# Kernel tuning notes

Hardware: AMD Instinct MI355X
Metric: run time of the kernel (lower is better)

Reference implementation:

```python
import jax, jax.numpy as jnp
import numpy as np

HEADS = 8
EMBED = 512
D_K = EMBED // HEADS
B, S = 2, 4096


def setup_inputs() -> dict:
    key = jax.random.key(0)
    ks = jax.random.split(key, 12)
    sc = 1.0 / np.sqrt(EMBED)
    inp = {
        "query": jax.random.normal(ks[0], (B, S, EMBED), jnp.float32),
        "key": jax.random.normal(ks[1], (B, S, EMBED), jnp.float32),
        "value": jax.random.normal(ks[2], (B, S, EMBED), jnp.float32),
        # causal (decoder) mask, broadcast over batch and heads
        "mask": jnp.tril(jnp.ones((S, S), jnp.int32))[None, None, :, :],
        "Wq": jax.random.normal(ks[3], (EMBED, EMBED), jnp.float32) * sc,
        "bq": jnp.zeros((EMBED,), jnp.float32),
        "Wk": jax.random.normal(ks[4], (EMBED, EMBED), jnp.float32) * sc,
        "bk": jnp.zeros((EMBED,), jnp.float32),
        "Wv": jax.random.normal(ks[5], (EMBED, EMBED), jnp.float32) * sc,
        "bv": jnp.zeros((EMBED,), jnp.float32),
        "Wo": jax.random.normal(ks[6], (EMBED, EMBED), jnp.float32) * sc,
        "bo": jnp.zeros((EMBED,), jnp.float32),
    }
    return inp


def reference(query, key, value, mask, Wq, bq, Wk, bk, Wv, bv, Wo, bo):
    b, s, e = query.shape
    # linear projections (torch Linear: x @ W.T + b)
    q = query @ Wq.T + bq
    k = key @ Wk.T + bk
    v = value @ Wv.T + bv
    # [b, h, s, d_k]
    q = q.reshape(b, s, HEADS, D_K).transpose(0, 2, 1, 3)
    k = k.reshape(b, s, HEADS, D_K).transpose(0, 2, 1, 3)
    v = v.reshape(b, s, HEADS, D_K).transpose(0, 2, 1, 3)
    scores = jnp.einsum("bhqd,bhkd->bhqk", q, k) / jnp.sqrt(jnp.float32(D_K))
    scores = jnp.where(mask == 0, jnp.float32(-1e20), scores)
    attn = jax.nn.softmax(scores, axis=-1)  # dropout is identity in eval
    ctx = jnp.einsum("bhqk,bhkd->bhqd", attn, v)
    ctx = ctx.transpose(0, 2, 1, 3).reshape(b, s, e)
    return ctx @ Wo.T + bo
```

## Files before the change

### kernel.cpp

```cpp
#include <hip/hip_runtime.h>
#include <hip/hip_bf16.h>

#define HEADS 8
#define DK    64
#define SEQ   4096
#define EMB   512
#define BATCH 2

using f32x4  = __attribute__((ext_vector_type(4))) float;
using f32x16 = __attribute__((ext_vector_type(16))) float;
using bf16x8 = __attribute__((ext_vector_type(8))) short;
using uint2v = __attribute__((ext_vector_type(2))) uint;

union frg { uint u[4]; bf16x8 v; };

__device__ __forceinline__ ushort f2bf(float f) {
    union { float f; uint32_t u; } x{f};
    uint32_t r = (x.u + 0x7fff + ((x.u >> 16) & 1)) >> 16;
    return (ushort)r;
}

__device__ __forceinline__ float bf2f(ushort u) {
    union { uint u; float f; } x; x.u = ((uint)u) << 16; return x.f;
}

__device__ __forceinline__ uint pk2(float a, float b) {
    __hip_bfloat162 h = __float22bfloat162_rn(make_float2(a, b));
    union { __hip_bfloat162 h; uint u; } c; c.h = h; return c.u;
}

__device__ __forceinline__ uint2v pswap(uint a, uint b) {
    return __builtin_amdgcn_permlane32_swap(a, b, false, false);
}

__device__ __forceinline__ void gld16(const ushort* g, short* l) {
    __builtin_amdgcn_global_load_lds(
        (const __attribute__((address_space(1))) void*)g,
        (__attribute__((address_space(3))) void*)l, 16, 0, 0);
}

__global__ __launch_bounds__(256) void gemm_qkv(
    const float* __restrict__ Aq, const float* __restrict__ Ak, const float* __restrict__ Av,
    const float* __restrict__ Wq, const float* __restrict__ Wk, const float* __restrict__ Wv,
    const float* __restrict__ bq, const float* __restrict__ bk, const float* __restrict__ bv,
    ushort* __restrict__ Qb, ushort* __restrict__ Kb, ushort* __restrict__ Vb)
{
    const int z = blockIdx.z;
    const float* A    = z == 0 ? Aq : z == 1 ? Ak : Av;
    const float* W    = z == 0 ? Wq : z == 1 ? Wk : Wv;
    const float* bias = z == 0 ? bq : z == 1 ? bk : bv;
    ushort* out       = z == 0 ? Qb : z == 1 ? Kb : Vb;
    const float osc   = z == 0 ? 0.125f * 1.44269504089f : 1.0f;

    const int Kd = EMB;
    __shared__ short As[128][40];
    __shared__ short Bs[128][40];

    const int tid = threadIdx.x;
    const int wave = tid >> 6, lane = tid & 63;
    const int wm = wave >> 1, wn = wave & 1;
    const int lr = lane & 15, lg = lane >> 4;
    const int m0 = blockIdx.x * 128, n0 = blockIdx.y * 128;

    f32x4 acc[4][4] = {};

    for (int k0 = 0; k0 < Kd; k0 += 32) {
        #pragma unroll
        for (int i = 0; i < 4; ++i) {
            int idx4 = tid + i * 256;
            int r = idx4 >> 3, c = (idx4 & 7) * 4;
            float4 va = *(const float4*)(A + (size_t)(m0 + r) * Kd + k0 + c);
            ushort4 ha;
            ha.x = f2bf(va.x); ha.y = f2bf(va.y); ha.z = f2bf(va.z); ha.w = f2bf(va.w);
            *(ushort4*)(&As[r][c]) = ha;
            float4 vb2 = *(const float4*)(W + (size_t)(n0 + r) * Kd + k0 + c);
            ushort4 hb;
            hb.x = f2bf(vb2.x); hb.y = f2bf(vb2.y); hb.z = f2bf(vb2.z); hb.w = f2bf(vb2.w);
            *(ushort4*)(&Bs[r][c]) = hb;
        }
        __syncthreads();

        bf16x8 a[4], bfr[4];
        #pragma unroll
        for (int i = 0; i < 4; ++i)
            a[i] = *(const bf16x8*)(&As[wm * 64 + i * 16 + lr][lg * 8]);
        #pragma unroll
        for (int i = 0; i < 4; ++i)
            bfr[i] = *(const bf16x8*)(&Bs[wn * 64 + i * 16 + lr][lg * 8]);

        #pragma unroll
        for (int mi = 0; mi < 4; ++mi)
            #pragma unroll
            for (int ni = 0; ni < 4; ++ni)
                acc[mi][ni] = __builtin_amdgcn_mfma_f32_16x16x32_bf16(
                    a[mi], bfr[ni], acc[mi][ni], 0, 0, 0);
        __syncthreads();
    }

    #pragma unroll
    for (int ni = 0; ni < 4; ++ni) {
        const int n = n0 + wn * 64 + ni * 16 + lr;
        const float bv2 = bias[n];
        #pragma unroll
        for (int mi = 0; mi < 4; ++mi) {
            #pragma unroll
            for (int j = 0; j < 4; ++j) {
                const int mm = m0 + wm * 64 + mi * 16 + lg * 4 + j;
                float v = (acc[mi][ni][j] + bv2) * osc;
                const int b = mm >> 12, s = mm & (SEQ - 1);
                const int h = n >> 6,  d = n & (DK - 1);
                size_t off;
                if (z == 2) off = ((size_t)(b * HEADS + h) * DK  + d) * SEQ + s;
                else        off = ((size_t)(b * HEADS + h) * SEQ + s) * DK + d;
                out[off] = f2bf(v);
            }
        }
    }
}

__global__ __launch_bounds__(256) void gemm_out(
    const ushort* __restrict__ Ab, const float* __restrict__ W,
    const float* __restrict__ bias, float* __restrict__ out)
{
    const int N = EMB, Kd = EMB;
    __shared__ short As[128][40];
    __shared__ short Bs[128][40];

    const int tid = threadIdx.x;
    const int wave = tid >> 6, lane = tid & 63;
    const int wm = wave >> 1, wn = wave & 1;
    const int lr = lane & 15, lg = lane >> 4;
    const int m0 = blockIdx.x * 128, n0 = blockIdx.y * 128;

    f32x4 acc[4][4] = {};

    for (int k0 = 0; k0 < Kd; k0 += 32) {
        #pragma unroll
        for (int i = 0; i < 2; ++i) {
            int idx8 = tid + i * 256;
            int r = idx8 >> 2, c = (idx8 & 3) * 8;
            bf16x8 v = *(const bf16x8*)(Ab + (size_t)(m0 + r) * Kd + k0 + c);
            *(bf16x8*)(&As[r][c]) = v;
        }
        #pragma unroll
        for (int i = 0; i < 4; ++i) {
            int idx4 = tid + i * 256;
            int r = idx4 >> 3, c = (idx4 & 7) * 4;
            float4 v = *(const float4*)(W + (size_t)(n0 + r) * Kd + k0 + c);
            ushort4 hb;
            hb.x = f2bf(v.x); hb.y = f2bf(v.y); hb.z = f2bf(v.z); hb.w = f2bf(v.w);
            *(ushort4*)(&Bs[r][c]) = hb;
        }
        __syncthreads();

        bf16x8 a[4], bfr[4];
        #pragma unroll
        for (int i = 0; i < 4; ++i)
            a[i] = *(const bf16x8*)(&As[wm * 64 + i * 16 + lr][lg * 8]);
        #pragma unroll
        for (int i = 0; i < 4; ++i)
            bfr[i] = *(const bf16x8*)(&Bs[wn * 64 + i * 16 + lr][lg * 8]);

        #pragma unroll
        for (int mi = 0; mi < 4; ++mi)
            #pragma unroll
            for (int ni = 0; ni < 4; ++ni)
                acc[mi][ni] = __builtin_amdgcn_mfma_f32_16x16x32_bf16(
                    a[mi], bfr[ni], acc[mi][ni], 0, 0, 0);
        __syncthreads();
    }

    #pragma unroll
    for (int ni = 0; ni < 4; ++ni) {
        const int n = n0 + wn * 64 + ni * 16 + lr;
        const float bv = bias[n];
        #pragma unroll
        for (int mi = 0; mi < 4; ++mi)
            #pragma unroll
            for (int j = 0; j < 4; ++j) {
                const int mm = m0 + wm * 64 + mi * 16 + lg * 4 + j;
                out[(size_t)mm * N + n] = acc[mi][ni][j] + bv;
            }
    }
}

__global__ __launch_bounds__(256) void merge_ctx(
    const ushort* __restrict__ Opseg, const float* __restrict__ Lseg,
    ushort* __restrict__ ctx)
{
    const int idx = blockIdx.x * 256 + threadIdx.x;
    const int d8  = idx & 7;
    const int row = idx >> 3;
    const int bh  = row >> 12, s = row & (SEQ - 1);
    const int nseg = (2 * (s >> 7) + 2 + 15) >> 4;

    float acc[8] = {};
    float l = 0.f;
    for (int g = 0; g < nseg; ++g) {
        const ushort* p = Opseg + (((size_t)g * 16 + bh) * SEQ + s) * 64 + d8 * 8;
        ushort4 a = *(const ushort4*)(p);
        ushort4 b2 = *(const ushort4*)(p + 4);
        acc[0] += bf2f(a.x);  acc[1] += bf2f(a.y);
        acc[2] += bf2f(a.z);  acc[3] += bf2f(a.w);
        acc[4] += bf2f(b2.x); acc[5] += bf2f(b2.y);
        acc[6] += bf2f(b2.z); acc[7] += bf2f(b2.w);
        l += Lseg[((size_t)g * 16 + bh) * SEQ + s];
    }
    const float rl = 1.0f / l;
    const int b = bh >> 3, h = bh & 7;
    ushort* o = ctx + ((size_t)b * SEQ + s) * EMB + h * 64 + d8 * 8;
    ushort4 r0, r1;
    r0.x = f2bf(acc[0] * rl); r0.y = f2bf(acc[1] * rl);
    r0.z = f2bf(acc[2] * rl); r0.w = f2bf(acc[3] * rl);
    r1.x = f2bf(acc[4] * rl); r1.y = f2bf(acc[5] * rl);
    r1.z = f2bf(acc[6] * rl); r1.w = f2bf(acc[7] * rl);
    *(ushort4*)(o)     = r0;
    *(ushort4*)(o + 4) = r1;
}

__global__ __launch_bounds__(256) void attn12(
    const ushort* __restrict__ Q, const ushort* __restrict__ K,
    const ushort* __restrict__ Vt,
    ushort* __restrict__ Opseg, float* __restrict__ Lseg)
{
    __shared__ short kv[2][2][64][64];

    const int tid  = threadIdx.x;
    const int wave = tid >> 6, lane = tid & 63;
    const int ql = lane & 31, hi = lane >> 5;

    const int bid = blockIdx.x;
    const int xcd = bid & 7;
    const int idx = bid >> 3;
    const int p   = idx & 1;
    const int j   = idx >> 1;
    int qblk, seg;
    if (j < 32)      { qblk = 31 - (j >> 2);      seg = j & 3; }
    else if (j < 56) { int jj = j - 32; int d3 = jj / 3; qblk = 23 - d3; seg = jj - d3 * 3; }
    else if (j < 72) { int jj = j - 56; qblk = 15 - (jj >> 1); seg = jj & 1; }
    else             { qblk = 7 - (j - 72);       seg = 0; }
    const int bh = xcd * 2 + p;

    const int q0b = qblk * 128;
    const int q0w = q0b + wave * 32;
    const int qg  = q0w + ql;

    const int ntchunk = 2 * qblk + 2;
    const int t_begin = seg * 16;
    const int t_end   = min(t_begin + 16, ntchunk);
    const int ntw     = (q0w + 31) / 64 + 1;

    const ushort* Qp = Q  + ((size_t)bh * SEQ + q0w) * DK;
    const ushort* Kp = K  + (size_t)bh * SEQ * DK;
    const ushort* Vp = Vt + (size_t)bh * DK * SEQ;

    bf16x8 qf[4];
    #pragma unroll
    for (int ks = 0; ks < 4; ++ks)
        qf[ks] = *(const bf16x8*)(Qp + ql * DK + ks * 16 + hi * 8);

    bf16x8 ones;
    #pragma unroll
    for (int i = 0; i < 8; ++i) ones[i] = (short)0x3F80;

    f32x16 oa0 = {}, oa1 = {};
    f32x16 oaL = {};

    auto stage = [&](int buf, int t) {
        const int r0 = wave * 16;
        const int rr = lane >> 3;
        const int c  = lane & 7;
        #pragma unroll
        for (int i = 0; i < 2; ++i) {
            int row = r0 + i * 8 + rr;
            gld16(Kp + (size_t)(t * 64 + row) * DK + ((c ^ (row & 7)) << 3),
                  &kv[buf][0][r0 + i * 8][0]);
        }
        #pragma unroll
        for (int i = 0; i < 2; ++i) {
            int row = r0 + i * 8 + rr;
            gld16(Vp + (size_t)row * SEQ + t * 64 + ((c ^ (row & 7)) << 3),
                  &kv[buf][1][r0 + i * 8][0]);
        }
    };

    const int swz = (ql & 7) << 4;

    auto compute = [&](int buf, int kv0, bool masked) {
        const char* kb = (const char*)&kv[buf][0][0][0];
        const char* vb = (const char*)&kv[buf][1][0][0];

        f32x16 s0, s1;
        #pragma unroll
        for (int r = 0; r < 16; ++r) { s0[r] = -20.0f; s1[r] = -20.0f; }
        #pragma unroll
        for (int ks = 0; ks < 4; ++ks) {
            bf16x8 kf = *(const bf16x8*)(kb + ql * 128 + (((ks * 2 + hi) << 4) ^ swz));
            s0 = __builtin_amdgcn_mfma_f32_32x32x16_bf16(kf, qf[ks], s0, 0, 0, 0);
        }
        #pragma unroll
        for (int ks = 0; ks < 4; ++ks) {
            bf16x8 kf = *(const bf16x8*)(kb + (32 + ql) * 128 + (((ks * 2 + hi) << 4) ^ swz));
            s1 = __builtin_amdgcn_mfma_f32_32x32x16_bf16(kf, qf[ks], s1, 0, 0, 0);
        }

        if (masked) {
            #pragma unroll
            for (int r = 0; r < 16; ++r) {
                int kvg = kv0 + (r & 3) + 8 * (r >> 2) + 4 * hi;
                if (kvg      > qg) s0[r] = -3e38f;
                if (kvg + 32 > qg) s1[r] = -3e38f;
            }
        }

        #pragma unroll
        for (int r = 0; r < 16; ++r) {
            s0[r] = exp2f(s0[r]);
            s1[r] = exp2f(s1[r]);
        }

        frg f0, f1, f2, f3;
        {
            uint w01 = pk2(s0[0], s0[1]),   w23 = pk2(s0[2], s0[3]);
            uint w45 = pk2(s0[4], s0[5]),   w67 = pk2(s0[6], s0[7]);
            uint w89 = pk2(s0[8], s0[9]),   wab = pk2(s0[10], s0[11]);
            uint wcd = pk2(s0[12], s0[13]), wef = pk2(s0[14], s0[15]);
            uint2v p0 = pswap(w01, w45), p1 = pswap(w23, w67);
            uint2v p2 = pswap(w89, wcd), p3 = pswap(wab, wef);
            f0.u[0] = p0[0]; f0.u[1] = p1[0]; f0.u[2] = p0[1]; f0.u[3] = p1[1];
            f1.u[0] = p2[0]; f1.u[1] = p3[0]; f1.u[2] = p2[1]; f1.u[3] = p3[1];
        }
        {
            uint w01 = pk2(s1[0], s1[1]),   w23 = pk2(s1[2], s1[3]);
            uint w45 = pk2(s1[4], s1[5]),   w67 = pk2(s1[6], s1[7]);
            uint w89 = pk2(s1[8], s1[9]),   wab = pk2(s1[10], s1[11]);
            uint wcd = pk2(s1[12], s1[13]), wef = pk2(s1[14], s1[15]);
            uint2v p0 = pswap(w01, w45), p1 = pswap(w23, w67);
            uint2v p2 = pswap(w89, wcd), p3 = pswap(wab, wef);
            f2.u[0] = p0[0]; f2.u[1] = p1[0]; f2.u[2] = p0[1]; f2.u[3] = p1[1];
            f3.u[0] = p2[0]; f3.u[1] = p3[0]; f3.u[2] = p2[1]; f3.u[3] = p3[1];
        }

        #pragma unroll
        for (int sl = 0; sl < 4; ++sl) {
            const frg* fp = sl == 0 ? &f0 : sl == 1 ? &f1 : sl == 2 ? &f2 : &f3;
            bf16x8 v0 = *(const bf16x8*)(vb + ql * 128        + (((sl * 2 + hi) << 4) ^ swz));
            bf16x8 v1 = *(const bf16x8*)(vb + (32 + ql) * 128 + (((sl * 2 + hi) << 4) ^ swz));
            oa0 = __builtin_amdgcn_mfma_f32_32x32x16_bf16(v0, fp->v, oa0, 0, 0, 0);
            oa1 = __builtin_amdgcn_mfma_f32_32x32x16_bf16(v1, fp->v, oa1, 0, 0, 0);
            oaL = __builtin_amdgcn_mfma_f32_32x32x16_bf16(ones, fp->v, oaL, 0, 0, 0);
        }
    };

    stage(0, t_begin);
    int cur = 0;
    for (int t = t_begin; t < t_end; ++t) {
        if (t + 1 < t_end) {
            stage(cur ^ 1, t + 1);
            asm volatile("s_waitcnt vmcnt(8)" ::: "memory");
        } else {
            asm volatile("s_waitcnt vmcnt(0)" ::: "memory");
        }
        __builtin_amdgcn_sched_barrier(0);
        __builtin_amdgcn_s_barrier();
        if (t < ntw)
            compute(cur, t * 64, t == ntw - 1);
        __builtin_amdgcn_s_barrier();
        cur ^= 1;
    }

    ushort* orow = Opseg + (((size_t)seg * 16 + bh) * SEQ + qg) * 64;
    #pragma unroll
    for (int g = 0; g < 4; ++g) {
        ushort4 pk;
        pk.x = f2bf(oa0[g * 4 + 0]); pk.y = f2bf(oa0[g * 4 + 1]);
        pk.z = f2bf(oa0[g * 4 + 2]); pk.w = f2bf(oa0[g * 4 + 3]);
        *(ushort4*)(orow + g * 8 + hi * 4) = pk;
    }
    #pragma unroll
    for (int g = 0; g < 4; ++g) {
        ushort4 pk;
        pk.x = f2bf(oa1[g * 4 + 0]); pk.y = f2bf(oa1[g * 4 + 1]);
        pk.z = f2bf(oa1[g * 4 + 2]); pk.w = f2bf(oa1[g * 4 + 3]);
        *(ushort4*)(orow + 32 + g * 8 + hi * 4) = pk;
    }
    if (hi == 0)
        Lseg[((size_t)seg * 16 + bh) * SEQ + qg] = oaL[0];
}

extern "C" void kernel_launch(void* const* d_in, const int* in_sizes, int n_in,
                              void* d_out, int out_size, void* d_ws, size_t ws_size,
                              hipStream_t stream) {
    const float* query = (const float*)d_in[0];
    const float* key   = (const float*)d_in[1];
    const float* value = (const float*)d_in[2];
    const float* Wq = (const float*)d_in[4];
    const float* bq = (const float*)d_in[5];
    const float* Wk = (const float*)d_in[6];
    const float* bk = (const float*)d_in[7];
    const float* Wv = (const float*)d_in[8];
    const float* bv = (const float*)d_in[9];
    const float* Wo = (const float*)d_in[10];
    const float* bo = (const float*)d_in[11];

    const size_t MK = (size_t)BATCH * SEQ * EMB;
    ushort* Qb = (ushort*)d_ws;
    ushort* Kb = Qb + MK;
    ushort* Vb = Kb + MK;
    ushort* Opseg = Vb + MK;
    float*  Lseg  = (float*)(Opseg + (size_t)4 * 16 * SEQ * DK);
    ushort* Cb = Qb;

    gemm_qkv<<<dim3(64, 4, 3), 256, 0, stream>>>(query, key, value,
                                                 Wq, Wk, Wv, bq, bk, bv,
                                                 Qb, Kb, Vb);
    attn12<<<dim3(1280), 256, 0, stream>>>(Qb, Kb, Vb, Opseg, Lseg);
    merge_ctx<<<dim3(2048), 256, 0, stream>>>(Opseg, Lseg, Cb);
    gemm_out<<<dim3(64, 4), 256, 0, stream>>>(Cb, Wo, bo, (float*)d_out);
}
```

Measured before the change: 146.1 us.

## Fuse split-KV merge into output GEMM and load QKV fp32 tiles via LDS DMA

The separate merge_ctx kernel is removed; the output projection GEMM now sums the per-segment partial outputs and normalizers while loading its A tile, which saves one launch and the ctx round trip through memory. The QKV projection GEMM now streams fp32 tiles straight into XOR-swizzled shared memory with global_load_lds and converts them to bf16 when reading fragments. In exchange, each of the 4 column blocks of the output GEMM repeats the merge, and the merge loop inside the GEMM main loop adds latency there. The fp32 LDS tiles also double the shared memory footprint.

```diff
diff --git a/kernel.cpp b/kernel.cpp
--- a/kernel.cpp
+++ b/kernel.cpp
@@ -39,7 +39,13 @@
         (__attribute__((address_space(3))) void*)l, 16, 0, 0);
 }
 
-__global__ __launch_bounds__(256) void gemm_qkv(
+__device__ __forceinline__ void gld16f(const float* g, float* l) {
+    __builtin_amdgcn_global_load_lds(
+        (const __attribute__((address_space(1))) void*)g,
+        (__attribute__((address_space(3))) void*)l, 16, 0, 0);
+}
+
+__global__ __launch_bounds__(256) void gemm_qkv2(
     const float* __restrict__ Aq, const float* __restrict__ Ak, const float* __restrict__ Av,
     const float* __restrict__ Wq, const float* __restrict__ Wk, const float* __restrict__ Wv,
     const float* __restrict__ bq, const float* __restrict__ bk, const float* __restrict__ bv,
@@ -52,7 +58,90 @@
     ushort* out       = z == 0 ? Qb : z == 1 ? Kb : Vb;
     const float osc   = z == 0 ? 0.125f * 1.44269504089f : 1.0f;
 
-    const int Kd = EMB;
+    __shared__ __align__(16) float As[128][32];
+    __shared__ __align__(16) float Bs[128][32];
+
+    const int tid = threadIdx.x;
+    const int wave = tid >> 6, lane = tid & 63;
+    const int wm = wave >> 1, wn = wave & 1;
+    const int lr = lane & 15, lg = lane >> 4;
+    const int rr = lane >> 3, cc = lane & 7;
+    const int m0 = blockIdx.x * 128, n0 = blockIdx.y * 128;
+
+    f32x4 acc[4][4] = {};
+
+    for (int k0 = 0; k0 < EMB; k0 += 32) {
+        #pragma unroll
+        for (int i = 0; i < 4; ++i) {
+            int row = wave * 32 + i * 8 + rr;
+            gld16f(A + (size_t)(m0 + row) * EMB + k0 + ((cc ^ (row & 7)) << 2),
+                   &As[wave * 32 + i * 8][0]);
+            gld16f(W + (size_t)(n0 + row) * EMB + k0 + ((cc ^ (row & 7)) << 2),
+                   &Bs[wave * 32 + i * 8][0]);
+        }
+        asm volatile("s_waitcnt vmcnt(0)" ::: "memory");
+        __builtin_amdgcn_s_barrier();
+
+        const char* ab = (const char*)&As[0][0];
+        const char* bb = (const char*)&Bs[0][0];
+        bf16x8 a[4], b[4];
+        #pragma unroll
+        for (int i = 0; i < 4; ++i) {
+            int row = wm * 64 + i * 16 + lr;
+            f32x4 lo = *(const f32x4*)(ab + row * 128 + (((2 * lg) ^ (row & 7)) << 4));
+            f32x4 hi = *(const f32x4*)(ab + row * 128 + (((2 * lg + 1) ^ (row & 7)) << 4));
+            frg f;
+            f.u[0] = pk2(lo[0], lo[1]); f.u[1] = pk2(lo[2], lo[3]);
+            f.u[2] = pk2(hi[0], hi[1]); f.u[3] = pk2(hi[2], hi[3]);
+            a[i] = f.v;
+        }
+        #pragma unroll
+        for (int i = 0; i < 4; ++i) {
+            int row = wn * 64 + i * 16 + lr;
+            f32x4 lo = *(const f32x4*)(bb + row * 128 + (((2 * lg) ^ (row & 7)) << 4));
+            f32x4 hi = *(const f32x4*)(bb + row * 128 + (((2 * lg + 1) ^ (row & 7)) << 4));
+            frg f;
+            f.u[0] = pk2(lo[0], lo[1]); f.u[1] = pk2(lo[2], lo[3]);
+            f.u[2] = pk2(hi[0], hi[1]); f.u[3] = pk2(hi[2], hi[3]);
+            b[i] = f.v;
+        }
+
+        #pragma unroll
+        for (int mi = 0; mi < 4; ++mi)
+            #pragma unroll
+            for (int ni = 0; ni < 4; ++ni)
+                acc[mi][ni] = __builtin_amdgcn_mfma_f32_16x16x32_bf16(
+                    a[mi], b[ni], acc[mi][ni], 0, 0, 0);
+        __builtin_amdgcn_s_barrier();
+    }
+
+    #pragma unroll
+    for (int ni = 0; ni < 4; ++ni) {
+        const int n = n0 + wn * 64 + ni * 16 + lr;
+        const float bv2 = bias[n];
+        #pragma unroll
+        for (int mi = 0; mi < 4; ++mi) {
+            #pragma unroll
+            for (int j = 0; j < 4; ++j) {
+                const int mm = m0 + wm * 64 + mi * 16 + lg * 4 + j;
+                float v = (acc[mi][ni][j] + bv2) * osc;
+                const int b2 = mm >> 12, s = mm & (SEQ - 1);
+                const int h = n >> 6,  d = n & (DK - 1);
+                size_t off;
+                if (z == 2) off = ((size_t)(b2 * HEADS + h) * DK  + d) * SEQ + s;
+                else        off = ((size_t)(b2 * HEADS + h) * SEQ + s) * DK + d;
+                out[off] = f2bf(v);
+            }
+        }
+    }
+}
+
+__global__ __launch_bounds__(256) void gemm_out2(
+    const ushort* __restrict__ Opseg, const float* __restrict__ Lseg,
+    const float* __restrict__ W, const float* __restrict__ bias,
+    float* __restrict__ out)
+{
+    const int N = EMB, Kd = EMB;
     __shared__ short As[128][40];
     __shared__ short Bs[128][40];
 
@@ -61,76 +150,7 @@
     const int wm = wave >> 1, wn = wave & 1;
     const int lr = lane & 15, lg = lane >> 4;
     const int m0 = blockIdx.x * 128, n0 = blockIdx.y * 128;
-
-    f32x4 acc[4][4] = {};
-
-    for (int k0 = 0; k0 < Kd; k0 += 32) {
-        #pragma unroll
-        for (int i = 0; i < 4; ++i) {
-            int idx4 = tid + i * 256;
-            int r = idx4 >> 3, c = (idx4 & 7) * 4;
-            float4 va = *(const float4*)(A + (size_t)(m0 + r) * Kd + k0 + c);
-            ushort4 ha;
-            ha.x = f2bf(va.x); ha.y = f2bf(va.y); ha.z = f2bf(va.z); ha.w = f2bf(va.w);
-            *(ushort4*)(&As[r][c]) = ha;
-            float4 vb2 = *(const float4*)(W + (size_t)(n0 + r) * Kd + k0 + c);
-            ushort4 hb;
-            hb.x = f2bf(vb2.x); hb.y = f2bf(vb2.y); hb.z = f2bf(vb2.z); hb.w = f2bf(vb2.w);
-            *(ushort4*)(&Bs[r][c]) = hb;
-        }
-        __syncthreads();
-
-        bf16x8 a[4], bfr[4];
-        #pragma unroll
-        for (int i = 0; i < 4; ++i)
-            a[i] = *(const bf16x8*)(&As[wm * 64 + i * 16 + lr][lg * 8]);
-        #pragma unroll
-        for (int i = 0; i < 4; ++i)
-            bfr[i] = *(const bf16x8*)(&Bs[wn * 64 + i * 16 + lr][lg * 8]);
-
-        #pragma unroll
-        for (int mi = 0; mi < 4; ++mi)
-            #pragma unroll
-            for (int ni = 0; ni < 4; ++ni)
-                acc[mi][ni] = __builtin_amdgcn_mfma_f32_16x16x32_bf16(
-                    a[mi], bfr[ni], acc[mi][ni], 0, 0, 0);
-        __syncthreads();
-    }
-
-    #pragma unroll
-    for (int ni = 0; ni < 4; ++ni) {
-        const int n = n0 + wn * 64 + ni * 16 + lr;
-        const float bv2 = bias[n];
-        #pragma unroll
-        for (int mi = 0; mi < 4; ++mi) {
-            #pragma unroll
-            for (int j = 0; j < 4; ++j) {
-                const int mm = m0 + wm * 64 + mi * 16 + lg * 4 + j;
-                float v = (acc[mi][ni][j] + bv2) * osc;
-                const int b = mm >> 12, s = mm & (SEQ - 1);
-                const int h = n >> 6,  d = n & (DK - 1);
-                size_t off;
-                if (z == 2) off = ((size_t)(b * HEADS + h) * DK  + d) * SEQ + s;
-                else        off = ((size_t)(b * HEADS + h) * SEQ + s) * DK + d;
-                out[off] = f2bf(v);
-            }
-        }
-    }
-}
-
-__global__ __launch_bounds__(256) void gemm_out(
-    const ushort* __restrict__ Ab, const float* __restrict__ W,
-    const float* __restrict__ bias, float* __restrict__ out)
-{
-    const int N = EMB, Kd = EMB;
-    __shared__ short As[128][40];
-    __shared__ short Bs[128][40];
-
-    const int tid = threadIdx.x;
-    const int wave = tid >> 6, lane = tid & 63;
-    const int wm = wave >> 1, wn = wave & 1;
-    const int lr = lane & 15, lg = lane >> 4;
-    const int m0 = blockIdx.x * 128, n0 = blockIdx.y * 128;
+    const int nseg = (2 * ((m0 & (SEQ - 1)) >> 7) + 17) >> 4;
 
     f32x4 acc[4][4] = {};
 
@@ -139,8 +159,27 @@
         for (int i = 0; i < 2; ++i) {
             int idx8 = tid + i * 256;
             int r = idx8 >> 2, c = (idx8 & 3) * 8;
-            bf16x8 v = *(const bf16x8*)(Ab + (size_t)(m0 + r) * Kd + k0 + c);
-            *(bf16x8*)(&As[r][c]) = v;
+            int mm = m0 + r;
+            int bb = mm >> 12, ss = mm & (SEQ - 1);
+            int k = k0 + c;
+            int bh = bb * 8 + (k >> 6), d = k & 63;
+            float a8[8] = {};
+            float l = 0.f;
+            for (int g = 0; g < nseg; ++g) {
+                const ushort* p = Opseg + (((size_t)g * 16 + bh) * SEQ + ss) * 64 + d;
+                bf16x8 v = *(const bf16x8*)(p);
+                #pragma unroll
+                for (int j = 0; j < 8; ++j) a8[j] += bf2f((ushort)v[j]);
+                l += Lseg[((size_t)g * 16 + bh) * SEQ + ss];
+            }
+            const float rl = 1.0f / l;
+            ushort4 h0, h1;
+            h0.x = f2bf(a8[0] * rl); h0.y = f2bf(a8[1] * rl);
+            h0.z = f2bf(a8[2] * rl); h0.w = f2bf(a8[3] * rl);
+            h1.x = f2bf(a8[4] * rl); h1.y = f2bf(a8[5] * rl);
+            h1.z = f2bf(a8[6] * rl); h1.w = f2bf(a8[7] * rl);
+            *(ushort4*)(&As[r][c])     = h0;
+            *(ushort4*)(&As[r][c + 4]) = h1;
         }
         #pragma unroll
         for (int i = 0; i < 4; ++i) {
@@ -182,40 +221,6 @@
                 out[(size_t)mm * N + n] = acc[mi][ni][j] + bv;
             }
     }
-}
-
-__global__ __launch_bounds__(256) void merge_ctx(
-    const ushort* __restrict__ Opseg, const float* __restrict__ Lseg,
-    ushort* __restrict__ ctx)
-{
-    const int idx = blockIdx.x * 256 + threadIdx.x;
-    const int d8  = idx & 7;
-    const int row = idx >> 3;
-    const int bh  = row >> 12, s = row & (SEQ - 1);
-    const int nseg = (2 * (s >> 7) + 2 + 15) >> 4;
-
-    float acc[8] = {};
-    float l = 0.f;
-    for (int g = 0; g < nseg; ++g) {
-        const ushort* p = Opseg + (((size_t)g * 16 + bh) * SEQ + s) * 64 + d8 * 8;
-        ushort4 a = *(const ushort4*)(p);
-        ushort4 b2 = *(const ushort4*)(p + 4);
-        acc[0] += bf2f(a.x);  acc[1] += bf2f(a.y);
-        acc[2] += bf2f(a.z);  acc[3] += bf2f(a.w);
-        acc[4] += bf2f(b2.x); acc[5] += bf2f(b2.y);
-        acc[6] += bf2f(b2.z); acc[7] += bf2f(b2.w);
-        l += Lseg[((size_t)g * 16 + bh) * SEQ + s];
-    }
-    const float rl = 1.0f / l;
-    const int b = bh >> 3, h = bh & 7;
-    ushort* o = ctx + ((size_t)b * SEQ + s) * EMB + h * 64 + d8 * 8;
-    ushort4 r0, r1;
-    r0.x = f2bf(acc[0] * rl); r0.y = f2bf(acc[1] * rl);
-    r0.z = f2bf(acc[2] * rl); r0.w = f2bf(acc[3] * rl);
-    r1.x = f2bf(acc[4] * rl); r1.y = f2bf(acc[5] * rl);
-    r1.z = f2bf(acc[6] * rl); r1.w = f2bf(acc[7] * rl);
-    *(ushort4*)(o)     = r0;
-    *(ushort4*)(o + 4) = r1;
 }
 
 __global__ __launch_bounds__(256) void attn12(
@@ -409,12 +414,10 @@
     ushort* Vb = Kb + MK;
     ushort* Opseg = Vb + MK;
     float*  Lseg  = (float*)(Opseg + (size_t)4 * 16 * SEQ * DK);
-    ushort* Cb = Qb;
-
-    gemm_qkv<<<dim3(64, 4, 3), 256, 0, stream>>>(query, key, value,
-                                                 Wq, Wk, Wv, bq, bk, bv,
-                                                 Qb, Kb, Vb);
+
+    gemm_qkv2<<<dim3(64, 4, 3), 256, 0, stream>>>(query, key, value,
+                                                  Wq, Wk, Wv, bq, bk, bv,
+                                                  Qb, Kb, Vb);
     attn12<<<dim3(1280), 256, 0, stream>>>(Qb, Kb, Vb, Opseg, Lseg);
-    merge_ctx<<<dim3(2048), 256, 0, stream>>>(Opseg, Lseg, Cb);
-    gemm_out<<<dim3(64, 4), 256, 0, stream>>>(Cb, Wo, bo, (float*)d_out);
-}
+    gemm_out2<<<dim3(64, 4), 256, 0, stream>>>(Opseg, Lseg, Wo, bo, (float*)d_out);
+}
```

Measured after the change: 175.9 us. 1.2x slower.
